# Performance work log

Measured on AMD Instinct MI355X. Metric: run time of the kernel, lower is better.

Reference implementation:

```python
import jax, jax.numpy as jnp
import numpy as np

IN_F, OUT_F, NB = 4096, 4096, 8
BS = IN_F // NB  # 512


def setup_inputs() -> dict:
    key = jax.random.key(0)
    k1, k2, k3, k4 = jax.random.split(key, 4)
    weight = jax.random.normal(k1, (OUT_F, IN_F), dtype=jnp.float32) * 0.02
    bias = jax.random.normal(k2, (OUT_F,), dtype=jnp.float32) * 0.02
    x = jax.random.normal(k3, (4, 2048, IN_F), dtype=jnp.float32)
    R_blocks = jax.random.normal(k4, (NB, BS, BS), dtype=jnp.float32) * 0.1
    return {"weight": weight, "bias": bias, "x": x, "R_blocks": R_blocks, "layer_idx": 0}


def cayley_transform(A):
    # A: [nb, bs, bs]; Q = (I - A_skew) @ inv(I + A_skew + 1e-6 I)
    bs = A.shape[-1]
    I = jnp.eye(bs, dtype=A.dtype)
    A_skew = 0.5 * (A - jnp.swapaxes(A, -2, -1))
    return jnp.matmul(I - A_skew, jnp.linalg.inv(I + A_skew + 1e-6 * I))


def reference(weight, bias, x, R_blocks, layer_idx):
    R_ortho = cayley_transform(R_blocks)  # [nb, bs, bs]
    # weight @ block_diag(R) == per-block contraction on the in_features axis
    w = weight.reshape(OUT_F, NB, BS)
    tw = jnp.einsum('onb,nbc->onc', w, R_ortho).reshape(OUT_F, IN_F)
    # F.linear: x @ tw.T + bias
    out = jnp.einsum('bsi,oi->bso', x, tw) + bias
    return out
```

## Files before the change

kernel.cpp:

```cpp
#include <hip/hip_runtime.h>
#include <hip/hip_bf16.h>


typedef unsigned short u16;
typedef __attribute__((ext_vector_type(8))) __bf16 bf16x8;
typedef __attribute__((ext_vector_type(4))) float f32x4;
typedef __attribute__((ext_vector_type(8))) unsigned short u16x8;
typedef __attribute__((ext_vector_type(4))) unsigned short u16x4;

#define C0   1.000001f
#define C1Q  2.000001f
#define AS1 __attribute__((address_space(1)))
#define AS3 __attribute__((address_space(3)))

__device__ __forceinline__ u16 f2bf(float x) {
  union { float f; unsigned u; } v; v.f = x;
  return (u16)((v.u + 0x7fffu + ((v.u >> 16) & 1u)) >> 16);
}
__device__ __forceinline__ float bf2f(u16 h) {
  union { float f; unsigned u; } v; v.u = ((unsigned)h) << 16; return v.f;
}

__global__ __launch_bounds__(256) void k_build_M(const float* __restrict__ R,
                                                 u16* __restrict__ Mh,
                                                 u16* __restrict__ Ml) {
  __shared__ float t1[32][33];
  const int n = blockIdx.z;
  const int tr = blockIdx.y * 32, tc = blockIdx.x * 32;
  const int ly = threadIdx.x >> 5, lx = threadIdx.x & 31;
  const float* Rb = R + (size_t)n * 262144;
  float a[4];
#pragma unroll
  for (int i = 0; i < 4; ++i) {
    a[i] = Rb[(size_t)(tr + ly + i * 8) * 512 + tc + lx];
    t1[ly + i * 8][lx] = Rb[(size_t)(tc + ly + i * 8) * 512 + tr + lx];
  }
  __syncthreads();
#pragma unroll
  for (int i = 0; i < 4; ++i) {
    const int r = tr + ly + i * 8, c = tc + lx;
    float m = 0.5f * (a[i] - t1[lx][ly + i * 8]) + (r == c ? C0 : 0.0f);
    u16 h = f2bf(m);
    const size_t idx = (size_t)n * 262144 + (size_t)r * 512 + c;
    Mh[idx] = h;
    Ml[idx] = f2bf(m - bf2f(h));
  }
}

__global__ __launch_bounds__(1024) void k_frob_alpha(const u16* __restrict__ G4,
                                                     float* __restrict__ alpha) {
  __shared__ float red[16];
  const int n = blockIdx.x, tid = threadIdx.x;
  const u16* src = G4 + (size_t)n * 262144;
  float s = 0.f;
  for (int i = tid; i < 32768; i += 1024) {
    u16x8 v = reinterpret_cast<const u16x8*>(src)[i];
#pragma unroll
    for (int e = 0; e < 8; ++e) { float f = bf2f(v[e]); s += f * f; }
  }
  for (int off = 32; off; off >>= 1) s += __shfl_down(s, off, 64);
  if ((tid & 63) == 0) red[tid >> 6] = s;
  __syncthreads();
  if (tid == 0) {
    float t = 0.f;
    for (int q = 0; q < 16; ++q) t += red[q];
    float lam = powf(t, 0.125f);
    alpha[n] = 2.0f / (C0 * C0 + lam);
  }
}

__global__ __launch_bounds__(256) void k_init_X0(const u16* __restrict__ Mh,
                                                 const u16* __restrict__ Ml,
                                                 const float* __restrict__ alpha,
                                                 u16* __restrict__ X0,
                                                 u16* __restrict__ X0t) {
  int idx = blockIdx.x * 256 + threadIdx.x;
  int n = idx >> 18, r = (idx >> 9) & 511, c = idx & 511;
  float m = bf2f(Mh[idx]) + bf2f(Ml[idx]);
  float a = alpha[n];
  X0[idx]  = f2bf(a * ((r == c ? 2.0f * C0 : 0.0f) - m));
  X0t[idx] = f2bf(a * m);
}

#define BMM_FRAGS(rs)                                                          \
  bf16x8 a[2], b[2], al2[2], bl2[2];                                           \
  _Pragma("unroll")                                                            \
  for (int i = 0; i < 2; ++i) {                                                \
    const int fr = wr * 32 + i * 16 + c15;                                     \
    const int ia = (rs) * 2048 + fr * 32 + ((lk ^ (fr & 3)) * 8);              \
    a[i] = *reinterpret_cast<const bf16x8*>(&sA[ia]);                          \
    if constexpr (PROD3) al2[i] = *reinterpret_cast<const bf16x8*>(&sAl[ia]);  \
  }                                                                            \
  _Pragma("unroll")                                                            \
  for (int j = 0; j < 2; ++j) {                                                \
    const int fc = wc * 32 + j * 16 + c15;                                     \
    const int ib = (rs) * 2048 + fc * 32 + ((lk ^ (fc & 3)) * 8);              \
    b[j] = *reinterpret_cast<const bf16x8*>(&sB[ib]);                          \
    if constexpr (PROD3) bl2[j] = *reinterpret_cast<const bf16x8*>(&sBl[ib]);  \
  }                                                                            \
  _Pragma("unroll")                                                            \
  for (int i = 0; i < 2; ++i)                                                  \
    _Pragma("unroll")                                                          \
    for (int j = 0; j < 2; ++j) {                                              \
      acc[i][j] = __builtin_amdgcn_mfma_f32_16x16x32_bf16(a[i], b[j], acc[i][j], 0, 0, 0); \
      if constexpr (PROD3) {                                                   \
        acc[i][j] = __builtin_amdgcn_mfma_f32_16x16x32_bf16(a[i],   bl2[j], acc[i][j], 0, 0, 0); \
        acc[i][j] = __builtin_amdgcn_mfma_f32_16x16x32_bf16(al2[i], b[j],   acc[i][j], 0, 0, 0); \
      }                                                                        \
    }

#define BMM_WAIT(SEL)                                                          \
  if ((SEL) == 0) {                                                            \
    if constexpr (PROD3) asm volatile("s_waitcnt vmcnt(8)" ::: "memory");      \
    else                 asm volatile("s_waitcnt vmcnt(4)" ::: "memory");      \
  } else if ((SEL) == 1) {                                                     \
    if constexpr (PROD3) asm volatile("s_waitcnt vmcnt(4)" ::: "memory");      \
    else                 asm volatile("s_waitcnt vmcnt(2)" ::: "memory");      \
  } else {                                                                     \
    asm volatile("s_waitcnt vmcnt(0)" ::: "memory");                           \
  }

template <int PROD3, int DMODE, int OMODE>
__global__ __launch_bounds__(256)
void k_bmm(const u16* __restrict__ Ah, const u16* __restrict__ Al,
           const u16* __restrict__ Bh, const u16* __restrict__ Bl,
           const u16* __restrict__ Dh, const u16* __restrict__ Dl,
           u16* __restrict__ Cnh, u16* __restrict__ Cnl,
           u16* __restrict__ Cth, u16* __restrict__ Ctl,
           float cd, float cs) {
  __shared__ __align__(16) u16 sA[4 * 2048], sB[4 * 2048];
  __shared__ __align__(16) u16 sAl[PROD3 ? 4 * 2048 : 8];
  __shared__ __align__(16) u16 sBl[PROD3 ? 4 * 2048 : 8];
  const size_t zb = (size_t)blockIdx.z * 262144;
  const int tid = threadIdx.x, lane = tid & 63, wave = tid >> 6;
  const int m0 = blockIdx.y * 64, n0 = blockIdx.x * 64;
  const int wr = wave >> 1, wc = wave & 1;
  const int c15 = lane & 15, lk = lane >> 4;
  const int srow = tid >> 2;
  const int sg = (tid & 3) ^ (srow & 3);
  f32x4 acc[2][2] = {};
  const u16* pa = Ah + zb + (size_t)(m0 + srow) * 512 + sg * 8;
  const u16* pb = Bh + zb + (size_t)(n0 + srow) * 512 + sg * 8;
  const u16* pal = PROD3 ? Al + zb + (size_t)(m0 + srow) * 512 + sg * 8 : pa;
  const u16* pbl = PROD3 ? Bl + zb + (size_t)(n0 + srow) * 512 + sg * 8 : pb;

  int jn = 0, js = 0;
  auto STG = [&]() {
    if (jn < 16) {
      const int off = jn << 5;
      u16* da = sA + js * 2048 + tid * 8;
      u16* db = sB + js * 2048 + tid * 8;
      __builtin_amdgcn_global_load_lds((const AS1 void*)(pa + off), (AS3 void*)da, 16, 0, 0);
      __builtin_amdgcn_global_load_lds((const AS1 void*)(pb + off), (AS3 void*)db, 16, 0, 0);
      if constexpr (PROD3) {
        __builtin_amdgcn_global_load_lds((const AS1 void*)(pal + off),
                                         (AS3 void*)(sAl + js * 2048 + tid * 8), 16, 0, 0);
        __builtin_amdgcn_global_load_lds((const AS1 void*)(pbl + off),
                                         (AS3 void*)(sBl + js * 2048 + tid * 8), 16, 0, 0);
      }
    }
    ++jn; js = (js + 1) & 3;
  };

  STG(); STG();
  int rs = 0;
  for (int t = 0; t < 14; ++t) {
    STG();
    BMM_WAIT(0)
    __builtin_amdgcn_s_barrier();
    BMM_FRAGS(rs)
    rs = (rs + 1) & 3;
  }
  STG();
  BMM_WAIT(1)
  __builtin_amdgcn_s_barrier();
  { BMM_FRAGS(rs) }
  rs = (rs + 1) & 3;
  STG();
  BMM_WAIT(2)
  __builtin_amdgcn_s_barrier();
  { BMM_FRAGS(rs) }

#pragma unroll
  for (int i = 0; i < 2; ++i)
#pragma unroll
    for (int j = 0; j < 2; ++j) {
      const int rowb = m0 + wr * 32 + i * 16 + lk * 4;
      const int col  = n0 + wc * 32 + j * 16 + c15;
      u16 hv[4], lv[4];
#pragma unroll
      for (int r = 0; r < 4; ++r) {
        float val = cs * acc[i][j][r];
        if constexpr (DMODE >= 1) {
          float d = bf2f(Dh[zb + (size_t)(rowb + r) * 512 + col]);
          if constexpr (DMODE == 2) d += bf2f(Dl[zb + (size_t)(rowb + r) * 512 + col]);
          val += cd * d;
        }
        u16 h = f2bf(val);
        if constexpr (OMODE & 1) Cnh[zb + (size_t)(rowb + r) * 512 + col] = h;
        u16 l = 0;
        if constexpr (OMODE & 10) l = f2bf(val - bf2f(h));
        if constexpr (OMODE & 2) Cnl[zb + (size_t)(rowb + r) * 512 + col] = l;
        hv[r] = h; lv[r] = l;
      }
      if constexpr (OMODE & 4) {
        u16x4 v; v[0] = hv[0]; v[1] = hv[1]; v[2] = hv[2]; v[3] = hv[3];
        *reinterpret_cast<u16x4*>(&Cth[zb + (size_t)col * 512 + rowb]) = v;
      }
      if constexpr (OMODE & 8) {
        u16x4 v; v[0] = lv[0]; v[1] = lv[1]; v[2] = lv[2]; v[3] = lv[3];
        *reinterpret_cast<u16x4*>(&Ctl[zb + (size_t)col * 512 + rowb]) = v;
      }
    }
}

__global__ __launch_bounds__(256)
void k_twmm(const u16* __restrict__ W, const u16* __restrict__ Qt,
            u16* __restrict__ tw) {
  __shared__ __align__(16) u16 sA[4 * 2048], sB[4 * 2048];
  const int z = blockIdx.z;
  const size_t zb = (size_t)z * 262144;
  const int tid = threadIdx.x, lane = tid & 63, wave = tid >> 6;
  const int m0 = blockIdx.y * 64, n0 = blockIdx.x * 64;
  const int wr = wave >> 1, wc = wave & 1;
  const int c15 = lane & 15, lk = lane >> 4;
  const int srow = tid >> 2;
  const int sg = (tid & 3) ^ (srow & 3);
  f32x4 acc[2][2] = {};
  const u16* pa = W + (size_t)(m0 + srow) * 4096 + z * 512 + sg * 8;
  const u16* pb = Qt + zb + (size_t)(n0 + srow) * 512 + sg * 8;

  int jn = 0, js = 0;
  auto STG = [&]() {
    if (jn < 16) {
      const int off = jn << 5;
      __builtin_amdgcn_global_load_lds((const AS1 void*)(pa + off),
                                       (AS3 void*)(sA + js * 2048 + tid * 8), 16, 0, 0);
      __builtin_amdgcn_global_load_lds((const AS1 void*)(pb + off),
                                       (AS3 void*)(sB + js * 2048 + tid * 8), 16, 0, 0);
    }
    ++jn; js = (js + 1) & 3;
  };

#define TW_FRAGS(rs)                                                           \
  {                                                                            \
    bf16x8 a[2], b[2];                                                         \
    _Pragma("unroll")                                                          \
    for (int i = 0; i < 2; ++i) {                                              \
      const int fr = wr * 32 + i * 16 + c15;                                   \
      a[i] = *reinterpret_cast<const bf16x8*>(                                 \
          &sA[(rs) * 2048 + fr * 32 + ((lk ^ (fr & 3)) * 8)]);                 \
    }                                                                          \
    _Pragma("unroll")                                                          \
    for (int j = 0; j < 2; ++j) {                                              \
      const int fc = wc * 32 + j * 16 + c15;                                   \
      b[j] = *reinterpret_cast<const bf16x8*>(                                 \
          &sB[(rs) * 2048 + fc * 32 + ((lk ^ (fc & 3)) * 8)]);                 \
    }                                                                          \
    _Pragma("unroll")                                                          \
    for (int i = 0; i < 2; ++i)                                                \
      _Pragma("unroll")                                                        \
      for (int j = 0; j < 2; ++j)                                              \
        acc[i][j] = __builtin_amdgcn_mfma_f32_16x16x32_bf16(a[i], b[j], acc[i][j], 0, 0, 0); \
  }

  STG(); STG();
  int rs = 0;
  for (int t = 0; t < 14; ++t) {
    STG();
    asm volatile("s_waitcnt vmcnt(4)" ::: "memory");
    __builtin_amdgcn_s_barrier();
    TW_FRAGS(rs)
    rs = (rs + 1) & 3;
  }
  STG();
  asm volatile("s_waitcnt vmcnt(2)" ::: "memory");
  __builtin_amdgcn_s_barrier();
  TW_FRAGS(rs)
  rs = (rs + 1) & 3;
  STG();
  asm volatile("s_waitcnt vmcnt(0)" ::: "memory");
  __builtin_amdgcn_s_barrier();
  TW_FRAGS(rs)

#pragma unroll
  for (int i = 0; i < 2; ++i)
#pragma unroll
    for (int j = 0; j < 2; ++j) {
      const int rowb = m0 + wr * 32 + i * 16 + lk * 4;
      const int col  = z * 512 + n0 + wc * 32 + j * 16 + c15;
#pragma unroll
      for (int r = 0; r < 4; ++r)
        tw[(size_t)(rowb + r) * 4096 + col] = f2bf(acc[i][j][r]);
    }
}

__global__ __launch_bounds__(256) void k_f32_to_bf16(const float* __restrict__ in,
                                                     u16* __restrict__ out) {
  int idx = blockIdx.x * 256 + threadIdx.x;
  const float* src = in + (size_t)idx * 8;
  float4 f0 = *reinterpret_cast<const float4*>(src);
  float4 f1 = *reinterpret_cast<const float4*>(src + 4);
  u16x8 w;
  w[0] = f2bf(f0.x); w[1] = f2bf(f0.y); w[2] = f2bf(f0.z); w[3] = f2bf(f0.w);
  w[4] = f2bf(f1.x); w[5] = f2bf(f1.y); w[6] = f2bf(f1.z); w[7] = f2bf(f1.w);
  *reinterpret_cast<u16x8*>(out + (size_t)idx * 8) = w;
}

#define NSL 18

#define RD_A3(dst, MH)                                                         \
  _Pragma("unroll")                                                            \
  for (int m = 0; m < 4; ++m)                                                  \
    dst[m] = *reinterpret_cast<const bf16x8*>(                                 \
        &lds[aslot * 4096 + ((MH) * 64 + m * 16 + c15) * 32 + gsw * 8]);

#define RD_B3(dst)                                                             \
  _Pragma("unroll")                                                            \
  for (int n = 0; n < 4; ++n)                                                  \
    dst[n] = *reinterpret_cast<const bf16x8*>(                                 \
        &lds[bslot * 4096 + (bq64 + n * 16 + c15) * 32 + gsw * 8]);

#define MFMA16(afX, bfX, MH)                                                   \
  __builtin_amdgcn_s_setprio(1);                                               \
  _Pragma("unroll")                                                            \
  for (int m = 0; m < 4; ++m)                                                  \
    _Pragma("unroll")                                                          \
    for (int n = 0; n < 4; ++n)                                                \
      acc[(MH) * 4 + m][n] = __builtin_amdgcn_mfma_f32_16x16x32_bf16(          \
          afX[m], bfX[n], acc[(MH) * 4 + m][n], 0, 0, 0);                      \
  __builtin_amdgcn_s_setprio(0);

#define TILE32(WM)                                                             \
  {                                                                            \
    int aslot = s0 + wr;            if (aslot >= NSL) aslot -= NSL;            \
    int bslot = s0 + 2 + (wc >> 1); if (bslot >= NSL) bslot -= NSL;            \
    STAGE(); STAGE();                                                          \
    RD_B3(bfr)                                                                 \
    RD_A3(afA, 0)                                                              \
    MFMA16(afA, bfr, 0)                                                        \
    STAGE(); STAGE();                                                          \
    RD_A3(afB, 1)                                                              \
    MFMA16(afB, bfr, 1)                                                        \
    if ((WM) == 1) asm volatile("s_waitcnt vmcnt(8)" ::: "memory");            \
    if ((WM) == 2) asm volatile("s_waitcnt vmcnt(4)" ::: "memory");            \
    if ((WM) == 3) asm volatile("s_waitcnt vmcnt(0)" ::: "memory");            \
    if ((WM) != 0) {                                                           \
      __builtin_amdgcn_s_barrier();                                            \
      __builtin_amdgcn_sched_barrier(0);                                       \
    }                                                                          \
    s0 += 4; if (s0 >= NSL) s0 -= NSL;                                         \
  }

__global__ __launch_bounds__(512, 2)
void k_gemm256(const u16* __restrict__ A, const u16* __restrict__ B,
               const float* __restrict__ bias,
               float* __restrict__ C, int N, int K) {
  __shared__ __align__(16) u16 lds[NSL * 4096];
  const int tid = threadIdx.x, lane = tid & 63, wave = tid >> 6;
  int bid = blockIdx.y * gridDim.x + blockIdx.x;
  const int cpx = (gridDim.x * gridDim.y) >> 3;
  bid = (bid & 7) * cpx + (bid >> 3);
  const int nbx = N >> 8;
  const int bx = bid % nbx, by = bid / nbx;
  const int m0 = by << 8, n0 = bx << 8;
  const int wr = wave >> 2, wc = wave & 3;
  const int srow = tid >> 2;
  const int sgc  = (tid & 3) ^ ((srow >> 1) & 3);
  const int c15 = lane & 15, lq = lane >> 4;
  const int gsw = lq ^ ((c15 >> 1) & 3);
  const int bq64 = (wc & 1) * 64;
  const int NT = K >> 5;

  f32x4 acc[8][4] = {};
  bf16x8 afA[4], afB[4], bfr[4];

  int jn = 0, js = 0;
  auto STAGE = [&]() {
    if (jn < 4 * NT) {
      const int t = jn >> 2, q = jn & 3;
      const u16* srcb = (q < 2)
          ? A + (size_t)(m0 + q * 128 + srow) * (size_t)K
          : B + (size_t)(n0 + (q - 2) * 128 + srow) * (size_t)K;
      const u16* src = srcb + (t << 5) + sgc * 8;
      u16* dst = (u16*)lds + js * 4096 + tid * 8;
      __builtin_amdgcn_global_load_lds(
          (const AS1 void*)src, (AS3 void*)dst, 16, 0, 0);
    }
    ++jn; js = (js == NSL - 1) ? 0 : js + 1;
  };

#pragma unroll
  for (int i = 0; i < 12; ++i) STAGE();
  asm volatile("s_waitcnt vmcnt(8)" ::: "memory");
  __builtin_amdgcn_s_barrier();
  __builtin_amdgcn_sched_barrier(0);

  int s0 = 0;
  for (int tau = 0; tau < NT - 3; ++tau) {
    TILE32(1)
  }
  TILE32(2)
  TILE32(3)
  TILE32(0)

#pragma unroll
  for (int n = 0; n < 4; ++n) {
    const int col = n0 + wc * 64 + n * 16 + c15;
    const float bv = bias[col];
#pragma unroll
    for (int mi = 0; mi < 8; ++mi) {
      const int rowb = m0 + wr * 128 + mi * 16 + (lq << 2);
#pragma unroll
      for (int r = 0; r < 4; ++r)
        C[(size_t)(rowb + r) * N + col] = acc[mi][n][r] + bv;
    }
  }
}

extern "C" void kernel_launch(void* const* d_in, const int* in_sizes, int n_in,
                              void* d_out, int out_size, void* d_ws, size_t ws_size,
                              hipStream_t stream) {
  const float* W    = (const float*)d_in[0];
  const float* bias = (const float*)d_in[1];
  const float* x    = (const float*)d_in[2];
  const float* R    = (const float*)d_in[3];
  float* out = (float*)d_out;

  char* ws = (char*)d_ws;
  u16* x_bf = (u16*)(ws);
  u16* tw   = (u16*)(ws + 67108864);
  u16* W_bf = (u16*)(ws + 100663296);

  char* arena = (char*)d_out;
  auto slot = [&](int i) -> u16* { return (u16*)(arena + (size_t)i * 4194304); };
  u16 *Mh = slot(0), *Ml = slot(1);
  u16 *G = slot(2), *G2 = slot(3), *G4 = slot(4);
  u16 *Xa = slot(5), *Xat = slot(6), *Xb = slot(7), *Xbt = slot(8);
  u16 *Xbl = slot(9), *Xbtl = slot(10);
  u16 *Tt = slot(2);
  u16 *Tth = slot(3), *Ttl = slot(4);
  u16 *X6h = slot(5), *X6l = slot(6);
  u16 *X6th = slot(11), *X6tl = slot(12);
  u16 *Qt = slot(13);
  float* alpha = (float*)(arena + (size_t)15 * 4194304);

  const dim3 g8(8, 8, 8);
  const u16* NUL = nullptr;

  k_build_M<<<dim3(16, 16, 8), 256, 0, stream>>>(R, Mh, Ml);
  k_bmm<0, 0, 1><<<g8, 256, 0, stream>>>(Mh, NUL, Mh, NUL, NUL, NUL,
                                         G, nullptr, nullptr, nullptr, 0.f, 1.f);
  k_bmm<0, 0, 1><<<g8, 256, 0, stream>>>(G, NUL, G, NUL, NUL, NUL,
                                         G2, nullptr, nullptr, nullptr, 0.f, 1.f);
  k_bmm<0, 0, 1><<<g8, 256, 0, stream>>>(G2, NUL, G2, NUL, NUL, NUL,
                                         G4, nullptr, nullptr, nullptr, 0.f, 1.f);
  k_frob_alpha<<<8, 1024, 0, stream>>>(G4, alpha);
  k_init_X0<<<8192, 256, 0, stream>>>(Mh, Ml, alpha, Xa, Xat);

  u16 *cur = Xa, *curt = Xat, *nxt = Xb, *nxtt = Xbt;
  for (int it = 0; it < 4; ++it) {
    k_bmm<0, 0, 4><<<g8, 256, 0, stream>>>(Mh, NUL, curt, NUL, NUL, NUL,
                                           nullptr, nullptr, Tt, nullptr, 0.f, 1.f);
    k_bmm<0, 1, 5><<<g8, 256, 0, stream>>>(cur, NUL, Tt, NUL, cur, NUL,
                                           nxt, nullptr, nxtt, nullptr, 2.f, -1.f);
    u16* t;
    t = cur; cur = nxt; nxt = t;
    t = curt; curt = nxtt; nxtt = t;
  }
  k_bmm<0, 0, 4><<<g8, 256, 0, stream>>>(Mh, NUL, curt, NUL, NUL, NUL,
                                         nullptr, nullptr, Tt, nullptr, 0.f, 1.f);
  k_bmm<0, 1, 15><<<g8, 256, 0, stream>>>(cur, NUL, Tt, NUL, cur, NUL,
                                          Xb, Xbl, Xbt, Xbtl, 2.f, -1.f);
  k_bmm<1, 0, 12><<<g8, 256, 0, stream>>>(Mh, Ml, Xbt, Xbtl, NUL, NUL,
                                          nullptr, nullptr, Tth, Ttl, 0.f, 1.f);
  k_bmm<1, 2, 15><<<g8, 256, 0, stream>>>(Xb, Xbl, Tth, Ttl, Xb, Xbl,
                                          X6h, X6l, X6th, X6tl, 2.f, -1.f);
  k_bmm<1, 2, 4><<<g8, 256, 0, stream>>>(Mh, Ml, X6th, X6tl, X6h, X6l,
                                         nullptr, nullptr, Qt, nullptr, C1Q, -1.f);
  k_f32_to_bf16<<<8192, 256, 0, stream>>>(W, W_bf);
  k_twmm<<<dim3(8, 64, 8), 256, 0, stream>>>(W_bf, Qt, tw);
  k_f32_to_bf16<<<16384, 256, 0, stream>>>(x, x_bf);
  k_gemm256<<<dim3(16, 32), 512, 0, stream>>>(x_bf, tw, bias, out, 4096, 4096);
}
```

Measured before the change: 550.6 us.

## Use scaled Newton-Schulz steps and fold fp32-to-bf16 casts into bmm grids

Replaces the plain Newton-Schulz inverse iteration with a scaled variant whose per-block coefficients are computed from the spectral estimate, which lets the low-precision loop run two iterations instead of four. The W and x fp32-to-bf16 conversions are spread over extra z-slices added to each small batched-matmul launch, so the conversion bandwidth overlaps with the under-occupied 8x8x8 bmm grids and two standalone kernels are removed. This cuts the serial chain of small kernels, at the cost of relying on the scaled iteration converging well enough for accuracy.

```diff
diff --git a/kernel.cpp b/kernel.cpp
--- a/kernel.cpp
+++ b/kernel.cpp
@@ -48,7 +48,9 @@
 }
 
 __global__ __launch_bounds__(1024) void k_frob_alpha(const u16* __restrict__ G4,
-                                                     float* __restrict__ alpha) {
+                                                     float* __restrict__ alpha,
+                                                     float* __restrict__ cdv,
+                                                     float* __restrict__ csv) {
   __shared__ float red[16];
   const int n = blockIdx.x, tid = threadIdx.x;
   const u16* src = G4 + (size_t)n * 262144;
@@ -66,6 +68,15 @@
     for (int q = 0; q < 16; ++q) t += red[q];
     float lam = powf(t, 0.125f);
     alpha[n] = 2.0f / (C0 * C0 + lam);
+    float e = (lam - C0 * C0) / (lam + C0 * C0);
+#pragma unroll
+    for (int k = 0; k < 3; ++k) {
+      float sq = e * e;
+      float c = 2.0f / (2.0f - sq);
+      cdv[k * 8 + n] = 2.0f * c;
+      csv[k * 8 + n] = -c;
+      e = sq / (2.0f - sq);
+    }
   }
 }
 
@@ -127,10 +138,29 @@
            const u16* __restrict__ Dh, const u16* __restrict__ Dl,
            u16* __restrict__ Cnh, u16* __restrict__ Cnl,
            u16* __restrict__ Cth, u16* __restrict__ Ctl,
-           float cd, float cs) {
+           float cd, float cs,
+           const float* __restrict__ cdp, const float* __restrict__ csp,
+           const float* __restrict__ cvsrc, u16* __restrict__ cvdst) {
   __shared__ __align__(16) u16 sA[4 * 2048], sB[4 * 2048];
   __shared__ __align__(16) u16 sAl[PROD3 ? 4 * 2048 : 8];
   __shared__ __align__(16) u16 sBl[PROD3 ? 4 * 2048 : 8];
+
+  if (blockIdx.z >= 8) {
+    const int zi = (blockIdx.z - 8) * 64 + blockIdx.y * 8 + blockIdx.x;
+    const int base = zi * 256 + (int)threadIdx.x;
+#pragma unroll
+    for (int e = 0; e < 16; ++e) {
+      const size_t g = (size_t)(base + e * 32768) * 8;
+      float4 f0 = *reinterpret_cast<const float4*>(cvsrc + g);
+      float4 f1 = *reinterpret_cast<const float4*>(cvsrc + g + 4);
+      u16x8 w;
+      w[0] = f2bf(f0.x); w[1] = f2bf(f0.y); w[2] = f2bf(f0.z); w[3] = f2bf(f0.w);
+      w[4] = f2bf(f1.x); w[5] = f2bf(f1.y); w[6] = f2bf(f1.z); w[7] = f2bf(f1.w);
+      *reinterpret_cast<u16x8*>(cvdst + g) = w;
+    }
+    return;
+  }
+
   const size_t zb = (size_t)blockIdx.z * 262144;
   const int tid = threadIdx.x, lane = tid & 63, wave = tid >> 6;
   const int m0 = blockIdx.y * 64, n0 = blockIdx.x * 64;
@@ -181,6 +211,8 @@
   __builtin_amdgcn_s_barrier();
   { BMM_FRAGS(rs) }
 
+  const float cdL = cdp ? cdp[blockIdx.z] : cd;
+  const float csL = csp ? csp[blockIdx.z] : cs;
 #pragma unroll
   for (int i = 0; i < 2; ++i)
 #pragma unroll
@@ -190,11 +222,11 @@
       u16 hv[4], lv[4];
 #pragma unroll
       for (int r = 0; r < 4; ++r) {
-        float val = cs * acc[i][j][r];
+        float val = csL * acc[i][j][r];
         if constexpr (DMODE >= 1) {
           float d = bf2f(Dh[zb + (size_t)(rowb + r) * 512 + col]);
           if constexpr (DMODE == 2) d += bf2f(Dl[zb + (size_t)(rowb + r) * 512 + col]);
-          val += cd * d;
+          val += cdL * d;
         }
         u16 h = f2bf(val);
         if constexpr (OMODE & 1) Cnh[zb + (size_t)(rowb + r) * 512 + col] = h;
@@ -295,18 +327,6 @@
     }
 }
 
-__global__ __launch_bounds__(256) void k_f32_to_bf16(const float* __restrict__ in,
-                                                     u16* __restrict__ out) {
-  int idx = blockIdx.x * 256 + threadIdx.x;
-  const float* src = in + (size_t)idx * 8;
-  float4 f0 = *reinterpret_cast<const float4*>(src);
-  float4 f1 = *reinterpret_cast<const float4*>(src + 4);
-  u16x8 w;
-  w[0] = f2bf(f0.x); w[1] = f2bf(f0.y); w[2] = f2bf(f0.z); w[3] = f2bf(f0.w);
-  w[4] = f2bf(f1.x); w[5] = f2bf(f1.y); w[6] = f2bf(f1.z); w[7] = f2bf(f1.w);
-  *reinterpret_cast<u16x8*>(out + (size_t)idx * 8) = w;
-}
-
 #define NSL 18
 
 #define RD_A3(dst, MH)                                                         \
@@ -444,42 +464,62 @@
   u16 *X6th = slot(11), *X6tl = slot(12);
   u16 *Qt = slot(13);
   float* alpha = (float*)(arena + (size_t)15 * 4194304);
-
-  const dim3 g8(8, 8, 8);
+  float* cdv = alpha + 8;
+  float* csv = alpha + 40;
+
+  const dim3 g8c(8, 8, 10);
   const u16* NUL = nullptr;
+  const float* NULF = nullptr;
+  auto cvs = [&](int i) -> const float* {
+    return i < 4 ? W + (size_t)i * 4194304 : x + (size_t)(i - 4) * 4194304;
+  };
+  auto cvd = [&](int i) -> u16* {
+    return i < 4 ? W_bf + (size_t)i * 4194304 : x_bf + (size_t)(i - 4) * 4194304;
+  };
 
   k_build_M<<<dim3(16, 16, 8), 256, 0, stream>>>(R, Mh, Ml);
-  k_bmm<0, 0, 1><<<g8, 256, 0, stream>>>(Mh, NUL, Mh, NUL, NUL, NUL,
-                                         G, nullptr, nullptr, nullptr, 0.f, 1.f);
-  k_bmm<0, 0, 1><<<g8, 256, 0, stream>>>(G, NUL, G, NUL, NUL, NUL,
-                                         G2, nullptr, nullptr, nullptr, 0.f, 1.f);
-  k_bmm<0, 0, 1><<<g8, 256, 0, stream>>>(G2, NUL, G2, NUL, NUL, NUL,
-                                         G4, nullptr, nullptr, nullptr, 0.f, 1.f);
-  k_frob_alpha<<<8, 1024, 0, stream>>>(G4, alpha);
+  k_bmm<0, 0, 1><<<g8c, 256, 0, stream>>>(Mh, NUL, Mh, NUL, NUL, NUL,
+                                          G, nullptr, nullptr, nullptr,
+                                          0.f, 1.f, NULF, NULF, cvs(0), cvd(0));
+  k_bmm<0, 0, 1><<<g8c, 256, 0, stream>>>(G, NUL, G, NUL, NUL, NUL,
+                                          G2, nullptr, nullptr, nullptr,
+                                          0.f, 1.f, NULF, NULF, cvs(1), cvd(1));
+  k_bmm<0, 0, 1><<<g8c, 256, 0, stream>>>(G2, NUL, G2, NUL, NUL, NUL,
+                                          G4, nullptr, nullptr, nullptr,
+                                          0.f, 1.f, NULF, NULF, cvs(2), cvd(2));
+  k_frob_alpha<<<8, 1024, 0, stream>>>(G4, alpha, cdv, csv);
   k_init_X0<<<8192, 256, 0, stream>>>(Mh, Ml, alpha, Xa, Xat);
 
   u16 *cur = Xa, *curt = Xat, *nxt = Xb, *nxtt = Xbt;
-  for (int it = 0; it < 4; ++it) {
-    k_bmm<0, 0, 4><<<g8, 256, 0, stream>>>(Mh, NUL, curt, NUL, NUL, NUL,
-                                           nullptr, nullptr, Tt, nullptr, 0.f, 1.f);
-    k_bmm<0, 1, 5><<<g8, 256, 0, stream>>>(cur, NUL, Tt, NUL, cur, NUL,
-                                           nxt, nullptr, nxtt, nullptr, 2.f, -1.f);
+  for (int it = 0; it < 2; ++it) {
+    k_bmm<0, 0, 4><<<g8c, 256, 0, stream>>>(Mh, NUL, curt, NUL, NUL, NUL,
+                                            nullptr, nullptr, Tt, nullptr,
+                                            0.f, 1.f, NULF, NULF,
+                                            cvs(3 + 2 * it), cvd(3 + 2 * it));
+    k_bmm<0, 1, 5><<<g8c, 256, 0, stream>>>(cur, NUL, Tt, NUL, cur, NUL,
+                                            nxt, nullptr, nxtt, nullptr,
+                                            0.f, 0.f, cdv + it * 8, csv + it * 8,
+                                            cvs(4 + 2 * it), cvd(4 + 2 * it));
     u16* t;
     t = cur; cur = nxt; nxt = t;
     t = curt; curt = nxtt; nxtt = t;
   }
-  k_bmm<0, 0, 4><<<g8, 256, 0, stream>>>(Mh, NUL, curt, NUL, NUL, NUL,
-                                         nullptr, nullptr, Tt, nullptr, 0.f, 1.f);
-  k_bmm<0, 1, 15><<<g8, 256, 0, stream>>>(cur, NUL, Tt, NUL, cur, NUL,
-                                          Xb, Xbl, Xbt, Xbtl, 2.f, -1.f);
-  k_bmm<1, 0, 12><<<g8, 256, 0, stream>>>(Mh, Ml, Xbt, Xbtl, NUL, NUL,
-                                          nullptr, nullptr, Tth, Ttl, 0.f, 1.f);
-  k_bmm<1, 2, 15><<<g8, 256, 0, stream>>>(Xb, Xbl, Tth, Ttl, Xb, Xbl,
-                                          X6h, X6l, X6th, X6tl, 2.f, -1.f);
-  k_bmm<1, 2, 4><<<g8, 256, 0, stream>>>(Mh, Ml, X6th, X6tl, X6h, X6l,
-                                         nullptr, nullptr, Qt, nullptr, C1Q, -1.f);
-  k_f32_to_bf16<<<8192, 256, 0, stream>>>(W, W_bf);
+  k_bmm<0, 0, 4><<<g8c, 256, 0, stream>>>(Mh, NUL, curt, NUL, NUL, NUL,
+                                          nullptr, nullptr, Tt, nullptr,
+                                          0.f, 1.f, NULF, NULF, cvs(7), cvd(7));
+  k_bmm<0, 1, 15><<<g8c, 256, 0, stream>>>(cur, NUL, Tt, NUL, cur, NUL,
+                                           Xb, Xbl, Xbt, Xbtl,
+                                           0.f, 0.f, cdv + 16, csv + 16,
+                                           cvs(8), cvd(8));
+  k_bmm<1, 0, 12><<<g8c, 256, 0, stream>>>(Mh, Ml, Xbt, Xbtl, NUL, NUL,
+                                           nullptr, nullptr, Tth, Ttl,
+                                           0.f, 1.f, NULF, NULF, cvs(9), cvd(9));
+  k_bmm<1, 2, 15><<<g8c, 256, 0, stream>>>(Xb, Xbl, Tth, Ttl, Xb, Xbl,
+                                           X6h, X6l, X6th, X6tl,
+                                           2.f, -1.f, NULF, NULF, cvs(10), cvd(10));
+  k_bmm<1, 2, 4><<<g8c, 256, 0, stream>>>(Mh, Ml, X6th, X6tl, X6h, X6l,
+                                          nullptr, nullptr, Qt, nullptr,
+                                          C1Q, -1.f, NULF, NULF, cvs(11), cvd(11));
   k_twmm<<<dim3(8, 64, 8), 256, 0, stream>>>(W_bf, Qt, tw);
-  k_f32_to_bf16<<<16384, 256, 0, stream>>>(x, x_bf);
   k_gemm256<<<dim3(16, 32), 512, 0, stream>>>(x_bf, tw, bias, out, 4096, 4096);
 }
```

New measurement: 541.6 us. No clear change (-1.6%).

## Replace Newton-Schulz inverse iterations with scaled polynomial steps and fuse fp32->bf16 conversions into bmm

Applied to the files above, without the earlier changes.

The matrix inverse for the Cayley transform now uses scaled Newton-Schulz style updates with per-block coefficients derived from the spectral bound, which cuts the number of sequential bmm launches. The first step is built from G and G2, and two independent products are batched into one launch through a DUAL mode. The W and x fp32-to-bf16 conversions are folded into extra z-blocks of the small, latency-bound bmm launches so they fill idle compute units, and the standalone conversion kernels are removed. This risks changing numerical accuracy, because the coefficients come from a crude norm estimate, and it uses more workspace slots in the output buffer.

```diff
diff --git a/kernel.cpp b/kernel.cpp
--- a/kernel.cpp
+++ b/kernel.cpp
@@ -48,7 +48,7 @@
 }
 
 __global__ __launch_bounds__(1024) void k_frob_alpha(const u16* __restrict__ G4,
-                                                     float* __restrict__ alpha) {
+                                                     float* __restrict__ coef) {
   __shared__ float red[16];
   const int n = blockIdx.x, tid = threadIdx.x;
   const u16* src = G4 + (size_t)n * 262144;
@@ -65,21 +65,40 @@
     float t = 0.f;
     for (int q = 0; q < 16; ++q) t += red[q];
     float lam = powf(t, 0.125f);
-    alpha[n] = 2.0f / (C0 * C0 + lam);
-  }
-}
-
-__global__ __launch_bounds__(256) void k_init_X0(const u16* __restrict__ Mh,
-                                                 const u16* __restrict__ Ml,
-                                                 const float* __restrict__ alpha,
-                                                 u16* __restrict__ X0,
-                                                 u16* __restrict__ X0t) {
+    float a = 2.0f / (C0 * C0 + lam);
+    coef[n] = a;
+    float e = (lam - C0 * C0) / (lam + C0 * C0);
+    float sq = e * e;
+    float c1 = 2.0f / (2.0f - sq);
+    coef[8 + n]  = 2.0f * c1;
+    coef[16 + n] = -c1 * a;
+    coef[24 + n] = 2.0f * c1 * a;
+    coef[32 + n] = -c1 * a * a;
+    e = sq / (2.0f - sq);
+    sq = e * e;
+    float c2 = 2.0f / (2.0f - sq);
+    coef[40 + n] = 2.0f * c2;
+    coef[48 + n] = -c2;
+    e = sq / (2.0f - sq);
+    sq = e * e;
+    float c3 = 2.0f / (2.0f - sq);
+    coef[56 + n] = 2.0f * c3;
+    coef[64 + n] = -c3;
+  }
+}
+
+__global__ __launch_bounds__(256) void k_init(const u16* __restrict__ Mh,
+                                              const u16* __restrict__ Ml,
+                                              const u16* __restrict__ G,
+                                              const u16* __restrict__ G2,
+                                              const float* __restrict__ coef,
+                                              u16* __restrict__ X0,
+                                              u16* __restrict__ T2) {
   int idx = blockIdx.x * 256 + threadIdx.x;
   int n = idx >> 18, r = (idx >> 9) & 511, c = idx & 511;
   float m = bf2f(Mh[idx]) + bf2f(Ml[idx]);
-  float a = alpha[n];
-  X0[idx]  = f2bf(a * ((r == c ? 2.0f * C0 : 0.0f) - m));
-  X0t[idx] = f2bf(a * m);
+  X0[idx] = f2bf(coef[n] * ((r == c ? 2.0f * C0 : 0.0f) - m));
+  T2[idx] = f2bf(coef[24 + n] * bf2f(G[idx]) + coef[32 + n] * bf2f(G2[idx]));
 }
 
 #define BMM_FRAGS(rs)                                                          \
@@ -120,18 +139,47 @@
     asm volatile("s_waitcnt vmcnt(0)" ::: "memory");                           \
   }
 
-template <int PROD3, int DMODE, int OMODE>
+template <int PROD3, int DMODE, int OMODE, int DUAL>
 __global__ __launch_bounds__(256)
 void k_bmm(const u16* __restrict__ Ah, const u16* __restrict__ Al,
            const u16* __restrict__ Bh, const u16* __restrict__ Bl,
            const u16* __restrict__ Dh, const u16* __restrict__ Dl,
            u16* __restrict__ Cnh, u16* __restrict__ Cnl,
            u16* __restrict__ Cth, u16* __restrict__ Ctl,
-           float cd, float cs) {
+           float cd, float cs,
+           const float* __restrict__ cdp, const float* __restrict__ csp,
+           const float* __restrict__ cvsrc, u16* __restrict__ cvdst, int zmm,
+           const u16* __restrict__ A2, const u16* __restrict__ B2,
+           const u16* __restrict__ D2, u16* __restrict__ C2) {
   __shared__ __align__(16) u16 sA[4 * 2048], sB[4 * 2048];
   __shared__ __align__(16) u16 sAl[PROD3 ? 4 * 2048 : 8];
   __shared__ __align__(16) u16 sBl[PROD3 ? 4 * 2048 : 8];
-  const size_t zb = (size_t)blockIdx.z * 262144;
+
+  if ((int)blockIdx.z >= zmm) {
+    const int zi = ((int)blockIdx.z - zmm) * 64 + blockIdx.y * 8 + blockIdx.x;
+    const int chunk = zi >> 7;
+    const int base = (zi & 127) * 256 + (int)threadIdx.x;
+    const float* src = cvsrc + (size_t)chunk * 4194304;
+    u16* dst = cvdst + (size_t)chunk * 4194304;
+#pragma unroll
+    for (int e = 0; e < 16; ++e) {
+      const size_t g = (size_t)(base + e * 32768) * 8;
+      float4 f0 = *reinterpret_cast<const float4*>(src + g);
+      float4 f1 = *reinterpret_cast<const float4*>(src + g + 4);
+      u16x8 w;
+      w[0] = f2bf(f0.x); w[1] = f2bf(f0.y); w[2] = f2bf(f0.z); w[3] = f2bf(f0.w);
+      w[4] = f2bf(f1.x); w[5] = f2bf(f1.y); w[6] = f2bf(f1.z); w[7] = f2bf(f1.w);
+      *reinterpret_cast<u16x8*>(dst + g) = w;
+    }
+    return;
+  }
+
+  const int zq = DUAL ? ((blockIdx.z >> 3) & 1) : 0;
+  const u16* Ah_ = (DUAL && zq) ? A2 : Ah;
+  const u16* Bh_ = (DUAL && zq) ? B2 : Bh;
+  const u16* Dh_ = (DUAL && zq) ? D2 : Dh;
+  u16* Cnh_ = (DUAL && zq) ? C2 : Cnh;
+  const size_t zb = (size_t)(blockIdx.z & 7) * 262144;
   const int tid = threadIdx.x, lane = tid & 63, wave = tid >> 6;
   const int m0 = blockIdx.y * 64, n0 = blockIdx.x * 64;
   const int wr = wave >> 1, wc = wave & 1;
@@ -139,8 +187,8 @@
   const int srow = tid >> 2;
   const int sg = (tid & 3) ^ (srow & 3);
   f32x4 acc[2][2] = {};
-  const u16* pa = Ah + zb + (size_t)(m0 + srow) * 512 + sg * 8;
-  const u16* pb = Bh + zb + (size_t)(n0 + srow) * 512 + sg * 8;
+  const u16* pa = Ah_ + zb + (size_t)(m0 + srow) * 512 + sg * 8;
+  const u16* pb = Bh_ + zb + (size_t)(n0 + srow) * 512 + sg * 8;
   const u16* pal = PROD3 ? Al + zb + (size_t)(m0 + srow) * 512 + sg * 8 : pa;
   const u16* pbl = PROD3 ? Bl + zb + (size_t)(n0 + srow) * 512 + sg * 8 : pb;
 
@@ -148,10 +196,10 @@
   auto STG = [&]() {
     if (jn < 16) {
       const int off = jn << 5;
-      u16* da = sA + js * 2048 + tid * 8;
-      u16* db = sB + js * 2048 + tid * 8;
-      __builtin_amdgcn_global_load_lds((const AS1 void*)(pa + off), (AS3 void*)da, 16, 0, 0);
-      __builtin_amdgcn_global_load_lds((const AS1 void*)(pb + off), (AS3 void*)db, 16, 0, 0);
+      __builtin_amdgcn_global_load_lds((const AS1 void*)(pa + off),
+                                       (AS3 void*)(sA + js * 2048 + tid * 8), 16, 0, 0);
+      __builtin_amdgcn_global_load_lds((const AS1 void*)(pb + off),
+                                       (AS3 void*)(sB + js * 2048 + tid * 8), 16, 0, 0);
       if constexpr (PROD3) {
         __builtin_amdgcn_global_load_lds((const AS1 void*)(pal + off),
                                          (AS3 void*)(sAl + js * 2048 + tid * 8), 16, 0, 0);
@@ -181,6 +229,8 @@
   __builtin_amdgcn_s_barrier();
   { BMM_FRAGS(rs) }
 
+  const float cdL = cdp ? cdp[blockIdx.z & 7] : cd;
+  const float csL = csp ? csp[blockIdx.z & 7] : cs;
 #pragma unroll
   for (int i = 0; i < 2; ++i)
 #pragma unroll
@@ -190,14 +240,14 @@
       u16 hv[4], lv[4];
 #pragma unroll
       for (int r = 0; r < 4; ++r) {
-        float val = cs * acc[i][j][r];
+        float val = csL * acc[i][j][r];
         if constexpr (DMODE >= 1) {
-          float d = bf2f(Dh[zb + (size_t)(rowb + r) * 512 + col]);
+          float d = bf2f(Dh_[zb + (size_t)(rowb + r) * 512 + col]);
           if constexpr (DMODE == 2) d += bf2f(Dl[zb + (size_t)(rowb + r) * 512 + col]);
-          val += cd * d;
+          val += cdL * d;
         }
         u16 h = f2bf(val);
-        if constexpr (OMODE & 1) Cnh[zb + (size_t)(rowb + r) * 512 + col] = h;
+        if constexpr (OMODE & 1) Cnh_[zb + (size_t)(rowb + r) * 512 + col] = h;
         u16 l = 0;
         if constexpr (OMODE & 10) l = f2bf(val - bf2f(h));
         if constexpr (OMODE & 2) Cnl[zb + (size_t)(rowb + r) * 512 + col] = l;
@@ -295,18 +345,6 @@
     }
 }
 
-__global__ __launch_bounds__(256) void k_f32_to_bf16(const float* __restrict__ in,
-                                                     u16* __restrict__ out) {
-  int idx = blockIdx.x * 256 + threadIdx.x;
-  const float* src = in + (size_t)idx * 8;
-  float4 f0 = *reinterpret_cast<const float4*>(src);
-  float4 f1 = *reinterpret_cast<const float4*>(src + 4);
-  u16x8 w;
-  w[0] = f2bf(f0.x); w[1] = f2bf(f0.y); w[2] = f2bf(f0.z); w[3] = f2bf(f0.w);
-  w[4] = f2bf(f1.x); w[5] = f2bf(f1.y); w[6] = f2bf(f1.z); w[7] = f2bf(f1.w);
-  *reinterpret_cast<u16x8*>(out + (size_t)idx * 8) = w;
-}
-
 #define NSL 18
 
 #define RD_A3(dst, MH)                                                         \
@@ -436,50 +474,48 @@
   auto slot = [&](int i) -> u16* { return (u16*)(arena + (size_t)i * 4194304); };
   u16 *Mh = slot(0), *Ml = slot(1);
   u16 *G = slot(2), *G2 = slot(3), *G4 = slot(4);
-  u16 *Xa = slot(5), *Xat = slot(6), *Xb = slot(7), *Xbt = slot(8);
-  u16 *Xbl = slot(9), *Xbtl = slot(10);
-  u16 *Tt = slot(2);
-  u16 *Tth = slot(3), *Ttl = slot(4);
-  u16 *X6h = slot(5), *X6l = slot(6);
-  u16 *X6th = slot(11), *X6tl = slot(12);
-  u16 *Qt = slot(13);
-  float* alpha = (float*)(arena + (size_t)15 * 4194304);
-
-  const dim3 g8(8, 8, 8);
+  u16 *X0 = slot(5), *T2 = slot(6), *X1 = slot(7), *X2 = slot(8), *T3 = slot(9);
+  u16 *X3h = slot(10), *X3l = slot(11), *X3th = slot(12), *X3tl = slot(13);
+  u16 *Tpth = slot(14), *Tptl = slot(15);
+  u16 *X4h = slot(16), *X4l = slot(17), *X4th = slot(18), *X4tl = slot(19);
+  u16 *Qt = slot(20);
+  float* coef = (float*)(arena + (size_t)21 * 4194304);
+
   const u16* NUL = nullptr;
+  const float* NULF = nullptr;
+  u16* NULW = nullptr;
+  const dim3 gC1(8, 8, 10);
+  const dim3 gC2(8, 8, 12);
 
   k_build_M<<<dim3(16, 16, 8), 256, 0, stream>>>(R, Mh, Ml);
-  k_bmm<0, 0, 1><<<g8, 256, 0, stream>>>(Mh, NUL, Mh, NUL, NUL, NUL,
-                                         G, nullptr, nullptr, nullptr, 0.f, 1.f);
-  k_bmm<0, 0, 1><<<g8, 256, 0, stream>>>(G, NUL, G, NUL, NUL, NUL,
-                                         G2, nullptr, nullptr, nullptr, 0.f, 1.f);
-  k_bmm<0, 0, 1><<<g8, 256, 0, stream>>>(G2, NUL, G2, NUL, NUL, NUL,
-                                         G4, nullptr, nullptr, nullptr, 0.f, 1.f);
-  k_frob_alpha<<<8, 1024, 0, stream>>>(G4, alpha);
-  k_init_X0<<<8192, 256, 0, stream>>>(Mh, Ml, alpha, Xa, Xat);
-
-  u16 *cur = Xa, *curt = Xat, *nxt = Xb, *nxtt = Xbt;
-  for (int it = 0; it < 4; ++it) {
-    k_bmm<0, 0, 4><<<g8, 256, 0, stream>>>(Mh, NUL, curt, NUL, NUL, NUL,
-                                           nullptr, nullptr, Tt, nullptr, 0.f, 1.f);
-    k_bmm<0, 1, 5><<<g8, 256, 0, stream>>>(cur, NUL, Tt, NUL, cur, NUL,
-                                           nxt, nullptr, nxtt, nullptr, 2.f, -1.f);
-    u16* t;
-    t = cur; cur = nxt; nxt = t;
-    t = curt; curt = nxtt; nxtt = t;
-  }
-  k_bmm<0, 0, 4><<<g8, 256, 0, stream>>>(Mh, NUL, curt, NUL, NUL, NUL,
-                                         nullptr, nullptr, Tt, nullptr, 0.f, 1.f);
-  k_bmm<0, 1, 15><<<g8, 256, 0, stream>>>(cur, NUL, Tt, NUL, cur, NUL,
-                                          Xb, Xbl, Xbt, Xbtl, 2.f, -1.f);
-  k_bmm<1, 0, 12><<<g8, 256, 0, stream>>>(Mh, Ml, Xbt, Xbtl, NUL, NUL,
-                                          nullptr, nullptr, Tth, Ttl, 0.f, 1.f);
-  k_bmm<1, 2, 15><<<g8, 256, 0, stream>>>(Xb, Xbl, Tth, Ttl, Xb, Xbl,
-                                          X6h, X6l, X6th, X6tl, 2.f, -1.f);
-  k_bmm<1, 2, 4><<<g8, 256, 0, stream>>>(Mh, Ml, X6th, X6tl, X6h, X6l,
-                                         nullptr, nullptr, Qt, nullptr, C1Q, -1.f);
-  k_f32_to_bf16<<<8192, 256, 0, stream>>>(W, W_bf);
+  k_bmm<0, 0, 1, 0><<<gC1, 256, 0, stream>>>(Mh, NUL, Mh, NUL, NUL, NUL,
+      G, NULW, NULW, NULW, 0.f, 1.f, NULF, NULF, W, W_bf, 8, NUL, NUL, NUL, NULW);
+  k_bmm<0, 0, 1, 0><<<gC1, 256, 0, stream>>>(G, NUL, G, NUL, NUL, NUL,
+      G2, NULW, NULW, NULW, 0.f, 1.f, NULF, NULF,
+      W + 4194304, W_bf + 4194304, 8, NUL, NUL, NUL, NULW);
+  k_bmm<0, 0, 1, 0><<<gC1, 256, 0, stream>>>(G2, NUL, G2, NUL, NUL, NUL,
+      G4, NULW, NULW, NULW, 0.f, 1.f, NULF, NULF,
+      W + 2 * 4194304, W_bf + 2 * 4194304, 8, NUL, NUL, NUL, NULW);
+  k_frob_alpha<<<8, 1024, 0, stream>>>(G4, coef);
+  k_init<<<8192, 256, 0, stream>>>(Mh, Ml, G, G2, coef, X0, T2);
+  k_bmm<0, 1, 1, 0><<<gC1, 256, 0, stream>>>(X0, NUL, G, NUL, X0, NUL,
+      X1, NULW, NULW, NULW, 0.f, 0.f, coef + 8, coef + 16,
+      W + 3 * 4194304, W_bf + 3 * 4194304, 8, NUL, NUL, NUL, NULW);
+  k_bmm<0, 1, 1, 1><<<dim3(8, 8, 20), 256, 0, stream>>>(X1, NUL, T2, NUL, X1, NUL,
+      X2, NULW, NULW, NULW, 0.f, 0.f, coef + 40, coef + 48,
+      x, x_bf, 16, T2, T2, T2, T3);
+  k_bmm<0, 1, 15, 0><<<gC2, 256, 0, stream>>>(X2, NUL, T3, NUL, X2, NUL,
+      X3h, X3l, X3th, X3tl, 0.f, 0.f, coef + 56, coef + 64,
+      x + (size_t)2 * 4194304, x_bf + (size_t)2 * 4194304, 8, NUL, NUL, NUL, NULW);
+  k_bmm<1, 0, 12, 0><<<gC2, 256, 0, stream>>>(Mh, Ml, X3th, X3tl, NUL, NUL,
+      NULW, NULW, Tpth, Tptl, 0.f, 1.f, NULF, NULF,
+      x + (size_t)4 * 4194304, x_bf + (size_t)4 * 4194304, 8, NUL, NUL, NUL, NULW);
+  k_bmm<1, 2, 15, 0><<<gC1, 256, 0, stream>>>(X3h, X3l, Tpth, Tptl, X3h, X3l,
+      X4h, X4l, X4th, X4tl, 2.f, -1.f, NULF, NULF,
+      x + (size_t)6 * 4194304, x_bf + (size_t)6 * 4194304, 8, NUL, NUL, NUL, NULW);
+  k_bmm<1, 2, 4, 0><<<gC1, 256, 0, stream>>>(Mh, Ml, X4th, X4tl, X4h, X4l,
+      NULW, NULW, Qt, NULW, C1Q, -1.f, NULF, NULF,
+      x + (size_t)7 * 4194304, x_bf + (size_t)7 * 4194304, 8, NUL, NUL, NUL, NULW);
   k_twmm<<<dim3(8, 64, 8), 256, 0, stream>>>(W_bf, Qt, tw);
-  k_f32_to_bf16<<<16384, 256, 0, stream>>>(x, x_bf);
   k_gemm256<<<dim3(16, 32), 512, 0, stream>>>(x_bf, tw, bias, out, 4096, 4096);
 }
```

After: 520.8 us. 1.06x faster.
